# Kernel tuning notes

Hardware: AMD Instinct MI355X
Metric: run time of the kernel (lower is better)

Reference implementation:

```python
import jax, jax.numpy as jnp
import numpy as np

B, T = 128, 2048
O, E, L = 128, 512, 34  # o_size, embed_dim, num_letter


def setup_inputs() -> dict:
    key = jax.random.key(0)
    ks = jax.random.split(key, 16)
    u = lambda k, shape, s: jax.random.uniform(k, shape, jnp.float32, -s, s)
    hk = jax.random.normal(ks[0], (B, T, O), jnp.float32)
    hv = jax.random.normal(ks[1], (B, T, O), jnp.float32)
    y_1 = jax.random.normal(ks[2], (B, E), jnp.float32)
    c_1 = jax.random.normal(ks[3], (B, O), jnp.float32)
    sh_1 = jax.random.normal(ks[4], (B, O), jnp.float32)
    sc_1 = jax.random.normal(ks[5], (B, O), jnp.float32)
    # valid-length mask (each row has at least T//2 valid positions)
    lengths = jax.random.randint(ks[6], (B,), T // 2, T + 1)
    mask = (jnp.arange(T)[None, :] < lengths[:, None]).astype(jnp.float32)
    s_rnn = 1.0 / np.sqrt(O)
    W_ih = u(ks[7], (4 * O, O + E), s_rnn)
    b_ih = u(ks[8], (4 * O,), s_rnn)
    W_hh = u(ks[9], (4 * O, O), s_rnn)
    b_hh = u(ks[10], (4 * O,), s_rnn)
    s1 = 1.0 / np.sqrt(O)
    W1 = u(ks[11], (L, O), s1); b1 = u(ks[12], (L,), s1)
    W2 = u(ks[13], (L, O), s1); b2 = u(ks[14], (L,), s1)
    s3 = 1.0 / np.sqrt(L)
    W3 = u(ks[15], (L, L), s3); b3 = u(jax.random.fold_in(key, 99), (L,), s3)
    return {"hk": hk, "hv": hv, "y_1": y_1, "c_1": c_1, "sh_1": sh_1,
            "sc_1": sc_1, "mask": mask, "W_ih": W_ih, "b_ih": b_ih,
            "W_hh": W_hh, "b_hh": b_hh, "W1": W1, "b1": b1,
            "W2": W2, "b2": b2, "W3": W3, "b3": b3}


def reference(hk, hv, y_1, c_1, sh_1, sc_1, mask,
              W_ih, b_ih, W_hh, b_hh, W1, b1, W2, b2, W3, b3):
    # LSTMCell (PyTorch gate order: i, f, g, o)
    x = jnp.concatenate([y_1, c_1], axis=1)            # [B, O+E]
    gates = x @ W_ih.T + b_ih + sh_1 @ W_hh.T + b_hh   # [B, 4O]
    i, f, g, o = jnp.split(gates, 4, axis=1)
    sc = jax.nn.sigmoid(f) * sc_1 + jax.nn.sigmoid(i) * jnp.tanh(g)
    sh = jax.nn.sigmoid(o) * jnp.tanh(sc)
    # attention scores keyed on cell state sc (faithful to source)
    scores = jnp.einsum('bto,bo->bt', hk, sc)          # [B, T]
    attn = jax.nn.softmax(scores, axis=1) * mask
    attn = attn / jnp.sum(attn, axis=1, keepdims=True)
    c = jnp.einsum('bt,bto->bo', attn, hv)             # [B, O]
    out = jax.nn.relu(sh @ W1.T + b1 + c @ W2.T + b2)
    out = jax.nn.softmax(out @ W3.T + b3, axis=1)      # [B, L]
    return (out, c, sh, sc)
```

## Files before the change

kernel.cpp:

```cpp
#include <hip/hip_runtime.h>
#include <math.h>

#define BB 128
#define TT 2048
#define OO 128
#define EE 512
#define LL 34
#define XDIM 640
#define SUBCH 64
#define SUB_LEN 32

__device__ __forceinline__ float sigmoidf_(float x) { return 1.0f / (1.0f + __expf(-x)); }

__global__ __launch_bounds__(256) void lstm_kernel(
    const float* __restrict__ y1, const float* __restrict__ c1,
    const float* __restrict__ sh1, const float* __restrict__ sc1,
    const float* __restrict__ Wih, const float* __restrict__ bih,
    const float* __restrict__ Whh, const float* __restrict__ bhh,
    float* __restrict__ out_sh, float* __restrict__ out_sc)
{
    __shared__ float xs[4][768];
    __shared__ float gbuf[4][4][16];
    const int tid = threadIdx.x;
    const int otile = blockIdx.x;
    const int qb = blockIdx.y * 4;

    for (int idx = tid; idx < 4 * 768; idx += 256) {
        int bi = idx / 768, k = idx - bi * 768;
        int b = qb + bi;
        float v;
        if (k < 512)      v = y1[b * EE + k];
        else if (k < 640) v = c1[b * OO + (k - 512)];
        else              v = sh1[b * OO + (k - 640)];
        xs[bi][k] = v;
    }
    __syncthreads();

    const int g = tid >> 6, l = tid & 63;
    #pragma unroll 2
    for (int i = 0; i < 16; ++i) {
        const int row = g * 128 + otile * 16 + i;
        const float* wr = Wih + (size_t)row * XDIM;
        float a0 = 0.f, a1 = 0.f, a2 = 0.f, a3 = 0.f;
        #pragma unroll
        for (int j = 0; j < 10; ++j) {
            float wv = wr[l + 64 * j];
            a0 += wv * xs[0][l + 64 * j];
            a1 += wv * xs[1][l + 64 * j];
            a2 += wv * xs[2][l + 64 * j];
            a3 += wv * xs[3][l + 64 * j];
        }
        const float* wh = Whh + (size_t)row * OO;
        #pragma unroll
        for (int j = 0; j < 2; ++j) {
            float wv = wh[l + 64 * j];
            a0 += wv * xs[0][640 + l + 64 * j];
            a1 += wv * xs[1][640 + l + 64 * j];
            a2 += wv * xs[2][640 + l + 64 * j];
            a3 += wv * xs[3][640 + l + 64 * j];
        }
        #pragma unroll
        for (int off = 32; off >= 1; off >>= 1) {
            a0 += __shfl_xor(a0, off);
            a1 += __shfl_xor(a1, off);
            a2 += __shfl_xor(a2, off);
            a3 += __shfl_xor(a3, off);
        }
        if (l == 0) {
            float bb = bih[row] + bhh[row];
            gbuf[g][0][i] = a0 + bb;
            gbuf[g][1][i] = a1 + bb;
            gbuf[g][2][i] = a2 + bb;
            gbuf[g][3][i] = a3 + bb;
        }
    }
    __syncthreads();

    if (tid < 64) {
        const int bi = tid >> 4, ol = tid & 15;
        const int b = qb + bi, o = otile * 16 + ol;
        float gi = gbuf[0][bi][ol], gf = gbuf[1][bi][ol];
        float gg = gbuf[2][bi][ol], go = gbuf[3][bi][ol];
        float sc = sigmoidf_(gf) * sc1[b * OO + o] + sigmoidf_(gi) * tanhf(gg);
        float sh = sigmoidf_(go) * tanhf(sc);
        out_sc[b * OO + o] = sc;
        out_sh[b * OO + o] = sh;
    }
}

__global__ __launch_bounds__(256, 2) void attn_kernel(
    const float* __restrict__ hk, const float* __restrict__ hv,
    const float* __restrict__ mask, const float* __restrict__ sc,
    float* __restrict__ ws_c, float2* __restrict__ pbuf)
{
    const int b = blockIdx.y;
    const int tid = threadIdx.x;
    const int wave = tid >> 6, lane = tid & 63;
    const int subchunk = blockIdx.x * 4 + wave;
    const int p = lane >> 5, q = lane & 31;
    const int r0 = subchunk * SUB_LEN;

    const float4 scq = *(const float4*)(sc + b * OO + q * 4);
    const float* mbase = mask + (size_t)b * TT + r0 + p;
    const float* kbase = hk + ((size_t)b * TT + r0 + p) * OO + q * 4;
    const float* vbase = hv + ((size_t)b * TT + r0 + p) * OO + q * 4;

    float mk[16];
    #pragma unroll
    for (int j = 0; j < 16; ++j) mk[j] = mbase[2 * j];

    float4 kv[16];
    #pragma unroll
    for (int j = 0; j < 16; ++j)
        kv[j] = *(const float4*)(kbase + (size_t)(2 * j) * OO);

    float d[16];
    #pragma unroll
    for (int j = 0; j < 16; ++j)
        d[j] = kv[j].x * scq.x + kv[j].y * scq.y + kv[j].z * scq.z + kv[j].w * scq.w;

    float4 vv[16];
    #pragma unroll
    for (int j = 0; j < 16; ++j)
        vv[j] = *(const float4*)(vbase + (size_t)(2 * j) * OO);

    #pragma unroll
    for (int j = 0; j < 16; ++j) {
        d[j] += __shfl_xor(d[j], 1);
        d[j] += __shfl_xor(d[j], 2);
        d[j] += __shfl_xor(d[j], 4);
        d[j] += __shfl_xor(d[j], 8);
        d[j] += __shfl_xor(d[j], 16);
    }
    float m = -INFINITY;
    #pragma unroll
    for (int j = 0; j < 16; ++j) if (mk[j] != 0.f) m = fmaxf(m, d[j]);
    m = fmaxf(m, __shfl_xor(m, 32));

    float e[16];
    float ps = 0.f;
    #pragma unroll
    for (int j = 0; j < 16; ++j) {
        e[j] = (mk[j] != 0.f) ? __expf(d[j] - m) : 0.f;
        ps += e[j];
    }
    ps += __shfl_xor(ps, 32);
    if (lane == 0)
        pbuf[(size_t)b * SUBCH + subchunk] = make_float2(m, ps);

    float4 acc = make_float4(0.f, 0.f, 0.f, 0.f);
    #pragma unroll
    for (int j = 0; j < 16; ++j) {
        acc.x += e[j] * vv[j].x;
        acc.y += e[j] * vv[j].y;
        acc.z += e[j] * vv[j].z;
        acc.w += e[j] * vv[j].w;
    }
    acc.x += __shfl_xor(acc.x, 32);
    acc.y += __shfl_xor(acc.y, 32);
    acc.z += __shfl_xor(acc.z, 32);
    acc.w += __shfl_xor(acc.w, 32);
    if (p == 0)
        *(float4*)(ws_c + ((size_t)b * SUBCH + subchunk) * OO + q * 4) = acc;
}

__global__ __launch_bounds__(256) void final_kernel(
    const float* __restrict__ ws_c, const float2* __restrict__ pbuf,
    const float* __restrict__ sh_in,
    const float* __restrict__ W1, const float* __restrict__ b1,
    const float* __restrict__ W2, const float* __restrict__ b2,
    const float* __restrict__ W3, const float* __restrict__ b3,
    float* __restrict__ out_p, float* __restrict__ out_c)
{
    const int b = blockIdx.x, tid = threadIdx.x;
    __shared__ float marr[SUBCH], Sarr[SUBCH], fac[SUBCH];
    __shared__ float cbuf[128], shbuf[128], h1[LL], zz[LL], red2[2];

    if (tid < SUBCH) {
        float2 p = pbuf[(size_t)b * SUBCH + tid];
        marr[tid] = p.x;
        Sarr[tid] = p.y;
    }
    __syncthreads();
    if (tid < SUBCH) {
        float M = marr[0];
        #pragma unroll
        for (int i = 1; i < SUBCH; ++i) M = fmaxf(M, marr[i]);
        float S = 0.f;
        #pragma unroll
        for (int i = 0; i < SUBCH; ++i) S += Sarr[i] * __expf(marr[i] - M);
        fac[tid] = __expf(marr[tid] - M) / S;
    }
    __syncthreads();

    if (tid < 128) {
        float s = 0.f;
        const float* base = ws_c + (size_t)b * SUBCH * OO + tid;
        #pragma unroll 8
        for (int i = 0; i < SUBCH; ++i) s += fac[i] * base[i * OO];
        cbuf[tid] = s;
        out_c[b * OO + tid] = s;
        shbuf[tid] = sh_in[b * OO + tid];
    }
    __syncthreads();

    const int o = tid >> 2, l2 = tid & 3;
    if (o < LL) {
        float a = 0.f;
        const float* w1r = W1 + o * OO;
        const float* w2r = W2 + o * OO;
        #pragma unroll 8
        for (int j = 0; j < 32; ++j) {
            int k = l2 + 4 * j;
            a += w1r[k] * shbuf[k] + w2r[k] * cbuf[k];
        }
        a += __shfl_xor(a, 1);
        a += __shfl_xor(a, 2);
        if (l2 == 0) h1[o] = fmaxf(a + b1[o] + b2[o], 0.f);
    }
    __syncthreads();

    if (o < LL) {
        float z = 0.f;
        const float* w3r = W3 + o * LL;
        for (int j = 0; j < 9; ++j) {
            int k = l2 + 4 * j;
            if (k < LL) z += w3r[k] * h1[k];
        }
        z += __shfl_xor(z, 1);
        z += __shfl_xor(z, 2);
        if (l2 == 0) zz[o] = z + b3[o];
    }
    __syncthreads();
    if (tid == 0) {
        float mm = zz[0];
        for (int i = 1; i < LL; i++) mm = fmaxf(mm, zz[i]);
        float ss = 0.f;
        for (int i = 0; i < LL; i++) ss += __expf(zz[i] - mm);
        red2[0] = mm; red2[1] = ss;
    }
    __syncthreads();
    if (tid < LL) out_p[b * LL + tid] = __expf(zz[tid] - red2[0]) / red2[1];
}

extern "C" void kernel_launch(void* const* d_in, const int* in_sizes, int n_in,
                              void* d_out, int out_size, void* d_ws, size_t ws_size,
                              hipStream_t stream) {
    (void)in_sizes; (void)n_in; (void)out_size; (void)ws_size;
    const float* hk   = (const float*)d_in[0];
    const float* hv   = (const float*)d_in[1];
    const float* y1   = (const float*)d_in[2];
    const float* c1   = (const float*)d_in[3];
    const float* sh1  = (const float*)d_in[4];
    const float* sc1  = (const float*)d_in[5];
    const float* mask = (const float*)d_in[6];
    const float* Wih  = (const float*)d_in[7];
    const float* bih  = (const float*)d_in[8];
    const float* Whh  = (const float*)d_in[9];
    const float* bhh  = (const float*)d_in[10];
    const float* W1   = (const float*)d_in[11];
    const float* b1   = (const float*)d_in[12];
    const float* W2   = (const float*)d_in[13];
    const float* b2   = (const float*)d_in[14];
    const float* W3   = (const float*)d_in[15];
    const float* b3   = (const float*)d_in[16];

    float* out    = (float*)d_out;
    float* out_c  = out + BB * LL;
    float* out_sh = out_c + BB * OO;
    float* out_sc = out_sh + BB * OO;

    float*  ws_c = (float*)d_ws;
    float2* pbuf = (float2*)(ws_c + (size_t)BB * SUBCH * OO);

    lstm_kernel<<<dim3(8, 32), 256, 0, stream>>>(y1, c1, sh1, sc1, Wih, bih, Whh, bhh,
                                                 out_sh, out_sc);
    attn_kernel<<<dim3(SUBCH / 4, BB), 256, 0, stream>>>(hk, hv, mask, out_sc, ws_c, pbuf);
    final_kernel<<<BB, 256, 0, stream>>>(ws_c, pbuf, out_sh, W1, b1, W2, b2, W3, b3,
                                         out, out_c);
}
```

Before: 337.8 us.

## Software-pipeline attention kernel over multiple subchunks per wave with K prefetch

```diff
diff --git a/kernel.cpp b/kernel.cpp
--- a/kernel.cpp
+++ b/kernel.cpp
@@ -9,6 +9,7 @@
 #define XDIM 640
 #define SUBCH 64
 #define SUB_LEN 32
+#define NT 4
 
 __device__ __forceinline__ float sigmoidf_(float x) { return 1.0f / (1.0f + __expf(-x)); }
 
@@ -96,72 +97,93 @@
     const int b = blockIdx.y;
     const int tid = threadIdx.x;
     const int wave = tid >> 6, lane = tid & 63;
-    const int subchunk = blockIdx.x * 4 + wave;
     const int p = lane >> 5, q = lane & 31;
-    const int r0 = subchunk * SUB_LEN;
 
     const float4 scq = *(const float4*)(sc + b * OO + q * 4);
-    const float* mbase = mask + (size_t)b * TT + r0 + p;
-    const float* kbase = hk + ((size_t)b * TT + r0 + p) * OO + q * 4;
-    const float* vbase = hv + ((size_t)b * TT + r0 + p) * OO + q * 4;
-
-    float mk[16];
-    #pragma unroll
-    for (int j = 0; j < 16; ++j) mk[j] = mbase[2 * j];
-
-    float4 kv[16];
+
+    const int sc0 = blockIdx.x * (NT * 4) + wave;
+    const size_t row0 = (size_t)b * TT + sc0 * SUB_LEN;
+    const float* kb = hk + (row0 + p) * OO + q * 4;
+    const float* vb = hv + (row0 + p) * OO + q * 4;
+    const float* mb = mask + row0;
+    const size_t adv = (size_t)4 * SUB_LEN * OO;
+
+    float4 K[16], V[16];
+
     #pragma unroll
     for (int j = 0; j < 16; ++j)
-        kv[j] = *(const float4*)(kbase + (size_t)(2 * j) * OO);
-
-    float d[16];
-    #pragma unroll
-    for (int j = 0; j < 16; ++j)
-        d[j] = kv[j].x * scq.x + kv[j].y * scq.y + kv[j].z * scq.z + kv[j].w * scq.w;
-
-    float4 vv[16];
-    #pragma unroll
-    for (int j = 0; j < 16; ++j)
-        vv[j] = *(const float4*)(vbase + (size_t)(2 * j) * OO);
-
-    #pragma unroll
-    for (int j = 0; j < 16; ++j) {
-        d[j] += __shfl_xor(d[j], 1);
-        d[j] += __shfl_xor(d[j], 2);
-        d[j] += __shfl_xor(d[j], 4);
-        d[j] += __shfl_xor(d[j], 8);
-        d[j] += __shfl_xor(d[j], 16);
-    }
-    float m = -INFINITY;
-    #pragma unroll
-    for (int j = 0; j < 16; ++j) if (mk[j] != 0.f) m = fmaxf(m, d[j]);
-    m = fmaxf(m, __shfl_xor(m, 32));
-
-    float e[16];
-    float ps = 0.f;
-    #pragma unroll
-    for (int j = 0; j < 16; ++j) {
-        e[j] = (mk[j] != 0.f) ? __expf(d[j] - m) : 0.f;
-        ps += e[j];
-    }
-    ps += __shfl_xor(ps, 32);
-    if (lane == 0)
-        pbuf[(size_t)b * SUBCH + subchunk] = make_float2(m, ps);
-
-    float4 acc = make_float4(0.f, 0.f, 0.f, 0.f);
-    #pragma unroll
-    for (int j = 0; j < 16; ++j) {
-        acc.x += e[j] * vv[j].x;
-        acc.y += e[j] * vv[j].y;
-        acc.z += e[j] * vv[j].z;
-        acc.w += e[j] * vv[j].w;
-    }
-    acc.x += __shfl_xor(acc.x, 32);
-    acc.y += __shfl_xor(acc.y, 32);
-    acc.z += __shfl_xor(acc.z, 32);
-    acc.w += __shfl_xor(acc.w, 32);
-    if (p == 0)
-        *(float4*)(ws_c + ((size_t)b * SUBCH + subchunk) * OO + q * 4) = acc;
+        K[j] = *(const float4*)(kb + (size_t)(2 * j) * OO);
+    __builtin_amdgcn_sched_barrier(0);
+
+    for (int t = 0; t < NT; ++t) {
+        const size_t toff = (size_t)t * adv;
+
+        const float* vbt = vb + toff;
+        #pragma unroll
+        for (int j = 0; j < 16; ++j)
+            V[j] = *(const float4*)(vbt + (size_t)(2 * j) * OO);
+        float mval = mb[t * (4 * SUB_LEN) + (lane & 31)];
+        __builtin_amdgcn_sched_barrier(0);
+
+        float d[16];
+        #pragma unroll
+        for (int j = 0; j < 16; ++j)
+            d[j] = K[j].x * scq.x + K[j].y * scq.y + K[j].z * scq.z + K[j].w * scq.w;
+        __builtin_amdgcn_sched_barrier(0);
+
+        if (t + 1 < NT) {
+            const float* kbt = kb + toff + adv;
+            #pragma unroll
+            for (int j = 0; j < 16; ++j)
+                K[j] = *(const float4*)(kbt + (size_t)(2 * j) * OO);
+        }
+        __builtin_amdgcn_sched_barrier(0);
+
+        #pragma unroll
+        for (int j = 0; j < 16; ++j) {
+            d[j] += __shfl_xor(d[j], 1);
+            d[j] += __shfl_xor(d[j], 2);
+            d[j] += __shfl_xor(d[j], 4);
+            d[j] += __shfl_xor(d[j], 8);
+            d[j] += __shfl_xor(d[j], 16);
+        }
+        float mk[16];
+        #pragma unroll
+        for (int j = 0; j < 16; ++j) mk[j] = __shfl(mval, 2 * j + p);
+
+        float m = -INFINITY;
+        #pragma unroll
+        for (int j = 0; j < 16; ++j) if (mk[j] != 0.f) m = fmaxf(m, d[j]);
+        m = fmaxf(m, __shfl_xor(m, 32));
+
+        float ps = 0.f;
+        #pragma unroll
+        for (int j = 0; j < 16; ++j) {
+            d[j] = (mk[j] != 0.f) ? __expf(d[j] - m) : 0.f;
+            ps += d[j];
+        }
+        ps += __shfl_xor(ps, 32);
+
+        const int subchunk = sc0 + t * 4;
+        if (lane == 0)
+            pbuf[(size_t)b * SUBCH + subchunk] = make_float2(m, ps);
+
+        float4 acc = make_float4(0.f, 0.f, 0.f, 0.f);
+        #pragma unroll
+        for (int j = 0; j < 16; ++j) {
+            acc.x += d[j] * V[j].x;
+            acc.y += d[j] * V[j].y;
+            acc.z += d[j] * V[j].z;
+            acc.w += d[j] * V[j].w;
+        }
+        acc.x += __shfl_xor(acc.x, 32);
+        acc.y += __shfl_xor(acc.y, 32);
+        acc.z += __shfl_xor(acc.z, 32);
+        acc.w += __shfl_xor(acc.w, 32);
+        if (p == 0)
+            *(float4*)(ws_c + ((size_t)b * SUBCH + subchunk) * OO + q * 4) = acc;
+        __builtin_amdgcn_sched_barrier(0);
+    }
 }
 
 __global__ __launch_bounds__(256) void final_kernel(
@@ -275,7 +297,8 @@
 
     lstm_kernel<<<dim3(8, 32), 256, 0, stream>>>(y1, c1, sh1, sc1, Wih, bih, Whh, bhh,
                                                  out_sh, out_sc);
-    attn_kernel<<<dim3(SUBCH / 4, BB), 256, 0, stream>>>(hk, hv, mask, out_sc, ws_c, pbuf);
+    attn_kernel<<<dim3(SUBCH / (4 * NT), BB), 256, 0, stream>>>(hk, hv, mask, out_sc,
+                                                                ws_c, pbuf);
     final_kernel<<<BB, 256, 0, stream>>>(ws_c, pbuf, out_sh, W1, b1, W2, b2, W3, b3,
                                          out, out_c);
 }
```

New measurement: 331.4 us. About the same (-1.9%).
